# Optimization experiments

Measured on AMD Instinct MI355X. Metric: run time of the kernel, lower is better.

## Reference

```python
import jax, jax.numpy as jnp
import numpy as np

N_DYADIC = 0   # dyadic refinement order (init kwarg n)
SOLVER = 0     # first-order explicit finite-difference scheme (init kwarg solver)


def _solve_goursat(inc):
    """Solve Goursat PDE K_{p+1,q+1} = K_{p+1,q} + K_{p,q+1} - K_{p,q} + inc[p,q]*K_{p,q}
    with boundary K[0,:] = K[:,0] = 1. inc: [B, P, Q] -> returns K[P,Q] per pair: [B]."""
    B, P, Q = inc.shape
    dt = inc.dtype
    ones_b = jnp.ones((B,), dt)

    def row_step(prev_row, inc_row):
        # prev_row: [B, Q+1] = K[p, :]; inc_row: [B, Q]
        def col_step(k_left, t):
            k_diag, k_up, a = t  # K[p,q], K[p,q+1], inc[p,q], each [B]
            k_new = k_up + (k_left - k_diag) + a * k_diag
            return k_new, k_new
        xs = (prev_row[:, :-1].T, prev_row[:, 1:].T, inc_row.T)  # [Q, B] each
        _, tail = jax.lax.scan(col_step, ones_b, xs)              # tail: [Q, B]
        new_row = jnp.concatenate([ones_b[:, None], tail.T], axis=1)
        return new_row, None

    final_row, _ = jax.lax.scan(row_step, jnp.ones((B, Q + 1), dt), jnp.swapaxes(inc, 0, 1))
    return final_row[:, -1]


def _sig_kernel_gram(X, Y, n=N_DYADIC):
    """Signature-kernel Gram matrix. X: [A, M, D], Y: [B, N, D] -> [A, B]."""
    dX = X[:, 1:, :] - X[:, :-1, :]          # [A, M-1, D]
    dY = Y[:, 1:, :] - Y[:, :-1, :]          # [B, N-1, D]
    Minc = jnp.einsum('apd,bqd->abpq', dX, dY)  # pairwise increment inner products
    f = 2 ** n
    if f > 1:  # dyadic grid refinement: split each cell into f*f subcells
        Minc = jnp.repeat(jnp.repeat(Minc, f, axis=2), f, axis=3) / (f * f)
    A, B, P, Q = Minc.shape
    K = _solve_goursat(Minc.reshape(A * B, P, Q))
    return K.reshape(A, B)


def setup_inputs() -> dict:
    key = jax.random.key(0)
    kx, ky = jax.random.split(key)
    SCALE = 0.05  # small Brownian-like increments keep the exponential kernel tame
    X = jnp.cumsum(SCALE * jax.random.normal(kx, (64, 128, 64), dtype=jnp.float32), axis=1)
    Y = jnp.cumsum(SCALE * jax.random.normal(ky, (64, 128, 64), dtype=jnp.float32), axis=1)
    return {"X": X, "Y": Y}


def reference(X, Y):
    K_XX = _sig_kernel_gram(X, X)
    K_YY = _sig_kernel_gram(Y, Y)
    K_XY = _sig_kernel_gram(X, Y)
    dist = jnp.mean(K_XX) + jnp.mean(K_YY) - 2.0 * jnp.mean(K_XY)
    return jnp.mean((X[:, 0, :] - Y[:, 0, :]) ** 2) + dist
```

## Files before the change

### kernel.cpp

```cpp
#include <hip/hip_runtime.h>
#include <math.h>

#define DD 64
#define MM 128
#define PSTR 66
#define PWORDS (16 * PSTR)

typedef float  f32x4v __attribute__((ext_vector_type(4)));
typedef __bf16 bf16x8 __attribute__((ext_vector_type(8)));

#define FOR8(F) F(0) F(1) F(2) F(3) F(4) F(5) F(6) F(7)

union FragU { unsigned int u[4]; bf16x8 v; };

__device__ __forceinline__ unsigned cvtpk(float lo, float hi) {
    unsigned r;
    asm("v_cvt_pk_bf16_f32 %0, %1, %2" : "=v"(r) : "v"(lo), "v"(hi));
    return r;
}

__device__ __forceinline__ float qswap(float x) {
    int t = __builtin_amdgcn_update_dpp(0, __float_as_int(x), 0xB1, 0xF, 0xF, true);
    return __int_as_float(t);
}

__device__ __forceinline__ bf16x8 dfrag_hi(const float* __restrict__ r0,
                                           const float* __restrict__ r1) {
    float4 a0 = *(const float4*)r0, a1 = *(const float4*)(r0 + 4);
    float4 b0 = *(const float4*)r1, b1 = *(const float4*)(r1 + 4);
    FragU f;
    f.u[0] = cvtpk(b0.x - a0.x, b0.y - a0.y);
    f.u[1] = cvtpk(b0.z - a0.z, b0.w - a0.w);
    f.u[2] = cvtpk(b1.x - a1.x, b1.y - a1.y);
    f.u[3] = cvtpk(b1.z - a1.z, b1.w - a1.w);
    return f.v;
}

template<int CTRL, int RM, bool BC>
__device__ __forceinline__ float dpp_add(float x) {
    int t = __builtin_amdgcn_update_dpp(0, __float_as_int(x), CTRL, RM, 0xf, BC);
    return x + __int_as_float(t);
}

__device__ __forceinline__ void scan4(float& x0, float& x1, float& x2, float& x3) {
#define LVL(CTRL, RM, BC) \
    x0 = dpp_add<CTRL, RM, BC>(x0); \
    x1 = dpp_add<CTRL, RM, BC>(x1); \
    x2 = dpp_add<CTRL, RM, BC>(x2); \
    x3 = dpp_add<CTRL, RM, BC>(x3);
    LVL(0x111, 0xf, true)
    LVL(0x112, 0xf, true)
    LVL(0x114, 0xf, true)
    LVL(0x118, 0xf, true)
    LVL(0x142, 0xa, false)
    LVL(0x143, 0xc, false)
#undef LVL
}

__global__ __launch_bounds__(64, 2) void sig_goursat_kernel(
        const float* __restrict__ X, const float* __restrict__ Y,
        float* __restrict__ Kout)
{
#define OFFB(bb) (((((bb) >> 2) + 1)) * (2 * ((bb) >> 2) + ((bb) & 3)))
    const int t = blockIdx.x;
    int g, b, j;
    if (t < 1088) {
        g = t < 544 ? 0 : 1;
        const int u = t - g * 544;
        int bb = (int)sqrtf(8.0f * (float)u + 1.0f);
        if (bb > 63) bb = 63;
        while (bb > 0  && OFFB(bb) > u) --bb;
        while (bb < 63 && OFFB(bb + 1) <= u) ++bb;
        b = bb;
        j = u - OFFB(bb);
    } else {
        const int u = t - 1088;
        g = 2; b = u & 63; j = u >> 6;
    }
    const int a0r = 4 * j, a1r = 4 * j + 1, a2r = 4 * j + 2, a3r = 4 * j + 3;
    const bool tri = (g < 2);
    const int a0 = (tri && a0r > b) ? b : a0r;
    const int a1 = (tri && a1r > b) ? b : a1r;
    const int a2 = (tri && a2r > b) ? b : a2r;
    const int a3 = (tri && a3r > b) ? b : a3r;

    const float* __restrict__ Ub = (g == 1 ? Y : X);
    const float* __restrict__ U0 = Ub + (size_t)a0 * (MM * DD);
    const float* __restrict__ U1 = Ub + (size_t)a1 * (MM * DD);
    const float* __restrict__ U2 = Ub + (size_t)a2 * (MM * DD);
    const float* __restrict__ U3 = Ub + (size_t)a3 * (MM * DD);
    const float* __restrict__ V  = (g == 0 ? X : Y) + (size_t)b * (MM * DD);

    const int lane = threadIdx.x;
    const int l15  = lane & 15;
    const int k8   = (lane >> 4) * 8;
    const int rowg = (lane >> 4) * 4;
    const int par  = l15 & 1;

    __shared__ unsigned incL[4 * PWORDS];
    unsigned* __restrict__ pl0 = incL;
    unsigned* __restrict__ pl1 = incL + PWORDS;
    unsigned* __restrict__ pl2 = incL + 2 * PWORDS;
    unsigned* __restrict__ pl3 = incL + 3 * PWORDS;

#define TBDECL(ct) bf16x8 tb0_##ct, tb1_##ct;
    FOR8(TBDECL)
#define TBUILD(ct) { int brow_ = ct * 16 + l15; if (brow_ > 126) brow_ = 126; \
        const float* vp_ = V + (size_t)brow_ * DD + k8; \
        tb0_##ct = dfrag_hi(vp_,      vp_ + DD); \
        tb1_##ct = dfrag_hi(vp_ + 32, vp_ + DD + 32); }
    FOR8(TBUILD)

    float KL0_0 = 1.f, KL1_0 = 1.f, KL0_1 = 1.f, KL1_1 = 1.f;
    float KL0_2 = 1.f, KL1_2 = 1.f, KL0_3 = 1.f, KL1_3 = 1.f;

    const int wA = (rowg + 2 * par) * PSTR + (l15 >> 1);
    const int wB = wA + PSTR;

#define CTSTEPS(ct) { \
        f32x4v c = {0.f, 0.f, 0.f, 0.f}; \
        c = __builtin_amdgcn_mfma_f32_16x16x32_bf16(ak0_, tb0_##ct, c, 0, 0, 0); \
        c = __builtin_amdgcn_mfma_f32_16x16x32_bf16(ak1_, tb1_##ct, c, 0, 0, 0); \
        const float n0 = qswap(c[0]); const float n1 = qswap(c[1]); \
        const float n2 = qswap(c[2]); const float n3 = qswap(c[3]); \
        const float loA = par ? n2 : c[0]; const float hiA = par ? c[2] : n0; \
        const float loB = par ? n3 : c[1]; const float hiB = par ? c[3] : n1; \
        pls[wA + (ct) * 8] = cvtpk(loA, hiA); \
        pls[wB + (ct) * 8] = cvtpk(loB, hiB); }

#define STAGE1(s) { \
        const float* ap_ = U##s + aoff; \
        bf16x8 ak0_ = dfrag_hi(ap_,      ap_ + DD); \
        bf16x8 ak1_ = dfrag_hi(ap_ + 32, ap_ + DD + 32); \
        unsigned* __restrict__ pls = pl##s; \
        FOR8(CTSTEPS) }

#define SQUAD(w0_, w1_, w2_, w3_) { \
        const float iE0 = __uint_as_float((w0_) << 16); \
        const float iO0 = __uint_as_float((w0_) & 0xffff0000u); \
        const float iE1 = __uint_as_float((w1_) << 16); \
        const float iO1 = __uint_as_float((w1_) & 0xffff0000u); \
        const float iE2 = __uint_as_float((w2_) << 16); \
        const float iO2 = __uint_as_float((w2_) & 0xffff0000u); \
        const float iE3 = __uint_as_float((w3_) << 16); \
        const float iO3 = __uint_as_float((w3_) & 0xffff0000u); \
        const float m00 = iE0 * KL0_0, m10 = iO0 * KL1_0; \
        const float m01 = iE1 * KL0_1, m11 = iO1 * KL1_1; \
        const float m02 = iE2 * KL0_2, m12 = iO2 * KL1_2; \
        const float m03 = iE3 * KL0_3, m13 = iO3 * KL1_3; \
        const float q0 = m00 + m10, q1 = m01 + m11; \
        const float q2 = m02 + m12, q3 = m03 + m13; \
        float s0 = q0, s1 = q1, s2 = q2, s3 = q3; \
        scan4(s0, s1, s2, s3); \
        const float ex0 = s0 - q0, ex1 = s1 - q1; \
        const float ex2 = s2 - q2, ex3 = s3 - q3; \
        KL1_0 += ex0 + m00;  KL0_0 += ex0; \
        KL1_1 += ex1 + m01;  KL0_1 += ex1; \
        KL1_2 += ex2 + m02;  KL0_2 += ex2; \
        KL1_3 += ex3 + m03;  KL0_3 += ex3; }

    const unsigned* __restrict__ pr0 = pl0 + lane;
    const unsigned* __restrict__ pr1 = pl1 + lane;
    const unsigned* __restrict__ pr2 = pl2 + lane;
    const unsigned* __restrict__ pr3 = pl3 + lane;

    for (int band = 0; band < 8; ++band) {
        int arow = band * 16 + l15; if (arow > 126) arow = 126;
        const size_t aoff = (size_t)arow * DD + k8;
        STAGE1(0) STAGE1(1) STAGE1(2) STAGE1(3)

        unsigned e0 = pr0[0],    e1 = pr1[0],    e2 = pr2[0],    e3 = pr3[0];
        unsigned f0 = pr0[PSTR], f1 = pr1[PSTR], f2 = pr2[PSTR], f3 = pr3[PSTR];
        #pragma unroll
        for (int r = 0; r < 13; ++r) {
            unsigned n0 = pr0[(r + 2) * PSTR];
            unsigned n1 = pr1[(r + 2) * PSTR];
            unsigned n2 = pr2[(r + 2) * PSTR];
            unsigned n3 = pr3[(r + 2) * PSTR];
            SQUAD(e0, e1, e2, e3)
            e0 = f0; e1 = f1; e2 = f2; e3 = f3;
            f0 = n0; f1 = n1; f2 = n2; f3 = n3;
        }
        if (band < 7) {
            unsigned n0 = pr0[15 * PSTR], n1 = pr1[15 * PSTR];
            unsigned n2 = pr2[15 * PSTR], n3 = pr3[15 * PSTR];
            SQUAD(e0, e1, e2, e3)
            e0 = f0; e1 = f1; e2 = f2; e3 = f3;
            f0 = n0; f1 = n1; f2 = n2; f3 = n3;
            SQUAD(e0, e1, e2, e3)
            SQUAD(f0, f1, f2, f3)
        } else {
            SQUAD(e0, e1, e2, e3)
            SQUAD(f0, f1, f2, f3)
        }
    }

    if (lane == 63) {
        float* kg = Kout + (size_t)g * 4096;
        kg[a0 * 64 + b] = KL1_0;
        if (!tri || a1r <= b) kg[a1 * 64 + b] = KL1_1;
        if (!tri || a2r <= b) kg[a2 * 64 + b] = KL1_2;
        if (!tri || a3r <= b) kg[a3 * 64 + b] = KL1_3;
    }
}

__global__ void sig_reduce_kernel(const float* __restrict__ X,
                                  const float* __restrict__ Y,
                                  const float* __restrict__ Kws,
                                  float* __restrict__ out)
{
    const int t = threadIdx.x;
    double accK = 0.0, acc2 = 0.0;
    for (int i = t; i < 4096; i += 256) {
        const int a = i >> 6, b = i & 63;
        if (a <= b) {
            const double w = (a == b) ? 1.0 : 2.0;
            accK += w * (double)Kws[i];
            accK += w * (double)Kws[4096 + i];
        }
        accK -= 2.0 * (double)Kws[8192 + i];
        const float df = X[(size_t)a * (MM * DD) + b] - Y[(size_t)a * (MM * DD) + b];
        acc2 += (double)df * (double)df;
    }
    __shared__ double red[256];
    red[t] = accK / 4096.0 + acc2 / 4096.0;
    __syncthreads();
    for (int s = 128; s > 0; s >>= 1) {
        if (t < s) red[t] += red[t + s];
        __syncthreads();
    }
    if (t == 0) out[0] = (float)red[0];
}

extern "C" void kernel_launch(void* const* d_in, const int* in_sizes, int n_in,
                              void* d_out, int out_size, void* d_ws, size_t ws_size,
                              hipStream_t stream) {
    const float* X = (const float*)d_in[0];
    const float* Y = (const float*)d_in[1];
    float* Kws = (float*)d_ws;
    float* out = (float*)d_out;

    sig_goursat_kernel<<<dim3(2112), dim3(64), 0, stream>>>(X, Y, Kws);
    sig_reduce_kernel<<<dim3(1), dim3(256), 0, stream>>>(X, Y, Kws, out);
}
```

Before: 131.5 us.

## Process two Goursat pairs per wave instead of four to double grid parallelism

Each 64-thread block now solves two (a,b) signature-kernel pairs instead of four, halving per-block registers and LDS and doubling the grid. The triangular mapping is recomputed for pairs of rows, with a duplicate flag on the odd diagonal. Launch bounds rise to four blocks per unit so more waves can overlap the serial DPP scan latency. In exchange, each V-fragment load and B-side MFMA operand build is amortised over fewer pairs, and per-pair latency is unchanged.

```diff
diff --git a/kernel.cpp b/kernel.cpp
--- a/kernel.cpp
+++ b/kernel.cpp
@@ -42,12 +42,10 @@
     return x + __int_as_float(t);
 }
 
-__device__ __forceinline__ void scan4(float& x0, float& x1, float& x2, float& x3) {
+__device__ __forceinline__ void scan2(float& x0, float& x1) {
 #define LVL(CTRL, RM, BC) \
     x0 = dpp_add<CTRL, RM, BC>(x0); \
-    x1 = dpp_add<CTRL, RM, BC>(x1); \
-    x2 = dpp_add<CTRL, RM, BC>(x2); \
-    x3 = dpp_add<CTRL, RM, BC>(x3);
+    x1 = dpp_add<CTRL, RM, BC>(x1);
     LVL(0x111, 0xf, true)
     LVL(0x112, 0xf, true)
     LVL(0x114, 0xf, true)
@@ -57,39 +55,33 @@
 #undef LVL
 }
 
-__global__ __launch_bounds__(64, 2) void sig_goursat_kernel(
+__global__ __launch_bounds__(64, 4) void sig_goursat_kernel(
         const float* __restrict__ X, const float* __restrict__ Y,
         float* __restrict__ Kout)
 {
-#define OFFB(bb) (((((bb) >> 2) + 1)) * (2 * ((bb) >> 2) + ((bb) & 3)))
-    const int t = blockIdx.x;
-    int g, b, j;
-    if (t < 1088) {
-        g = t < 544 ? 0 : 1;
-        const int u = t - g * 544;
-        int bb = (int)sqrtf(8.0f * (float)u + 1.0f);
-        if (bb > 63) bb = 63;
-        while (bb > 0  && OFFB(bb) > u) --bb;
-        while (bb < 63 && OFFB(bb + 1) <= u) ++bb;
-        b = bb;
-        j = u - OFFB(bb);
+    const int bid = blockIdx.x;
+    int g, a0, a1, bcol;
+    bool dup = false;
+    if (bid < 2112) {
+        g = bid < 1056 ? 0 : 1;
+        const int t = bid - g * 1056;
+        bcol = (int)(2.0f * sqrtf((float)t + 1.0f));
+        if (bcol > 63) bcol = 63;
+        while (bcol > 0  && ((bcol + 1) * (bcol + 1)) / 4 > t) --bcol;
+        while (bcol < 63 && ((bcol + 2) * (bcol + 2)) / 4 <= t) ++bcol;
+        const int j = t - ((bcol + 1) * (bcol + 1)) / 4;
+        a0 = 2 * j; a1 = 2 * j + 1;
+        if (a1 > bcol) { a1 = a0; dup = true; }
     } else {
-        const int u = t - 1088;
-        g = 2; b = u & 63; j = u >> 6;
-    }
-    const int a0r = 4 * j, a1r = 4 * j + 1, a2r = 4 * j + 2, a3r = 4 * j + 3;
-    const bool tri = (g < 2);
-    const int a0 = (tri && a0r > b) ? b : a0r;
-    const int a1 = (tri && a1r > b) ? b : a1r;
-    const int a2 = (tri && a2r > b) ? b : a2r;
-    const int a3 = (tri && a3r > b) ? b : a3r;
+        const int t = bid - 2112;
+        g = 2; bcol = t & 63;
+        a0 = (t >> 6) * 2; a1 = a0 + 1;
+    }
 
     const float* __restrict__ Ub = (g == 1 ? Y : X);
     const float* __restrict__ U0 = Ub + (size_t)a0 * (MM * DD);
     const float* __restrict__ U1 = Ub + (size_t)a1 * (MM * DD);
-    const float* __restrict__ U2 = Ub + (size_t)a2 * (MM * DD);
-    const float* __restrict__ U3 = Ub + (size_t)a3 * (MM * DD);
-    const float* __restrict__ V  = (g == 0 ? X : Y) + (size_t)b * (MM * DD);
+    const float* __restrict__ V  = (g == 0 ? X : Y) + (size_t)bcol * (MM * DD);
 
     const int lane = threadIdx.x;
     const int l15  = lane & 15;
@@ -97,11 +89,9 @@
     const int rowg = (lane >> 4) * 4;
     const int par  = l15 & 1;
 
-    __shared__ unsigned incL[4 * PWORDS];
+    __shared__ unsigned incL[2 * PWORDS];
     unsigned* __restrict__ pl0 = incL;
     unsigned* __restrict__ pl1 = incL + PWORDS;
-    unsigned* __restrict__ pl2 = incL + 2 * PWORDS;
-    unsigned* __restrict__ pl3 = incL + 3 * PWORDS;
 
 #define TBDECL(ct) bf16x8 tb0_##ct, tb1_##ct;
     FOR8(TBDECL)
@@ -111,8 +101,8 @@
         tb1_##ct = dfrag_hi(vp_ + 32, vp_ + DD + 32); }
     FOR8(TBUILD)
 
-    float KL0_0 = 1.f, KL1_0 = 1.f, KL0_1 = 1.f, KL1_1 = 1.f;
-    float KL0_2 = 1.f, KL1_2 = 1.f, KL0_3 = 1.f, KL1_3 = 1.f;
+    float KL0_0 = 1.f, KL1_0 = 1.f;
+    float KL0_1 = 1.f, KL1_1 = 1.f;
 
     const int wA = (rowg + 2 * par) * PSTR + (l15 >> 1);
     const int wB = wA + PSTR;
@@ -135,72 +125,53 @@
         unsigned* __restrict__ pls = pl##s; \
         FOR8(CTSTEPS) }
 
-#define SQUAD(w0_, w1_, w2_, w3_) { \
+#define SDUAL(w0_, w1_) { \
         const float iE0 = __uint_as_float((w0_) << 16); \
         const float iO0 = __uint_as_float((w0_) & 0xffff0000u); \
         const float iE1 = __uint_as_float((w1_) << 16); \
         const float iO1 = __uint_as_float((w1_) & 0xffff0000u); \
-        const float iE2 = __uint_as_float((w2_) << 16); \
-        const float iO2 = __uint_as_float((w2_) & 0xffff0000u); \
-        const float iE3 = __uint_as_float((w3_) << 16); \
-        const float iO3 = __uint_as_float((w3_) & 0xffff0000u); \
         const float m00 = iE0 * KL0_0, m10 = iO0 * KL1_0; \
         const float m01 = iE1 * KL0_1, m11 = iO1 * KL1_1; \
-        const float m02 = iE2 * KL0_2, m12 = iO2 * KL1_2; \
-        const float m03 = iE3 * KL0_3, m13 = iO3 * KL1_3; \
         const float q0 = m00 + m10, q1 = m01 + m11; \
-        const float q2 = m02 + m12, q3 = m03 + m13; \
-        float s0 = q0, s1 = q1, s2 = q2, s3 = q3; \
-        scan4(s0, s1, s2, s3); \
+        float s0 = q0, s1 = q1; \
+        scan2(s0, s1); \
         const float ex0 = s0 - q0, ex1 = s1 - q1; \
-        const float ex2 = s2 - q2, ex3 = s3 - q3; \
         KL1_0 += ex0 + m00;  KL0_0 += ex0; \
-        KL1_1 += ex1 + m01;  KL0_1 += ex1; \
-        KL1_2 += ex2 + m02;  KL0_2 += ex2; \
-        KL1_3 += ex3 + m03;  KL0_3 += ex3; }
+        KL1_1 += ex1 + m01;  KL0_1 += ex1; }
 
     const unsigned* __restrict__ pr0 = pl0 + lane;
     const unsigned* __restrict__ pr1 = pl1 + lane;
-    const unsigned* __restrict__ pr2 = pl2 + lane;
-    const unsigned* __restrict__ pr3 = pl3 + lane;
 
     for (int band = 0; band < 8; ++band) {
         int arow = band * 16 + l15; if (arow > 126) arow = 126;
         const size_t aoff = (size_t)arow * DD + k8;
-        STAGE1(0) STAGE1(1) STAGE1(2) STAGE1(3)
-
-        unsigned e0 = pr0[0],    e1 = pr1[0],    e2 = pr2[0],    e3 = pr3[0];
-        unsigned f0 = pr0[PSTR], f1 = pr1[PSTR], f2 = pr2[PSTR], f3 = pr3[PSTR];
+        STAGE1(0) STAGE1(1)
+
+        unsigned e0 = pr0[0],    e1 = pr1[0];
+        unsigned f0 = pr0[PSTR], f1 = pr1[PSTR];
         #pragma unroll
         for (int r = 0; r < 13; ++r) {
             unsigned n0 = pr0[(r + 2) * PSTR];
             unsigned n1 = pr1[(r + 2) * PSTR];
-            unsigned n2 = pr2[(r + 2) * PSTR];
-            unsigned n3 = pr3[(r + 2) * PSTR];
-            SQUAD(e0, e1, e2, e3)
-            e0 = f0; e1 = f1; e2 = f2; e3 = f3;
-            f0 = n0; f1 = n1; f2 = n2; f3 = n3;
+            SDUAL(e0, e1)
+            e0 = f0; e1 = f1; f0 = n0; f1 = n1;
         }
         if (band < 7) {
             unsigned n0 = pr0[15 * PSTR], n1 = pr1[15 * PSTR];
-            unsigned n2 = pr2[15 * PSTR], n3 = pr3[15 * PSTR];
-            SQUAD(e0, e1, e2, e3)
-            e0 = f0; e1 = f1; e2 = f2; e3 = f3;
-            f0 = n0; f1 = n1; f2 = n2; f3 = n3;
-            SQUAD(e0, e1, e2, e3)
-            SQUAD(f0, f1, f2, f3)
+            SDUAL(e0, e1)
+            e0 = f0; e1 = f1; f0 = n0; f1 = n1;
+            SDUAL(e0, e1)
+            SDUAL(f0, f1)
         } else {
-            SQUAD(e0, e1, e2, e3)
-            SQUAD(f0, f1, f2, f3)
+            SDUAL(e0, e1)
+            SDUAL(f0, f1)
         }
     }
 
     if (lane == 63) {
         float* kg = Kout + (size_t)g * 4096;
-        kg[a0 * 64 + b] = KL1_0;
-        if (!tri || a1r <= b) kg[a1 * 64 + b] = KL1_1;
-        if (!tri || a2r <= b) kg[a2 * 64 + b] = KL1_2;
-        if (!tri || a3r <= b) kg[a3 * 64 + b] = KL1_3;
+        kg[a0 * 64 + bcol] = KL1_0;
+        if (!dup) kg[a1 * 64 + bcol] = KL1_1;
     }
 }
 
@@ -240,6 +211,6 @@
     float* Kws = (float*)d_ws;
     float* out = (float*)d_out;
 
-    sig_goursat_kernel<<<dim3(2112), dim3(64), 0, stream>>>(X, Y, Kws);
+    sig_goursat_kernel<<<dim3(4160), dim3(64), 0, stream>>>(X, Y, Kws);
     sig_reduce_kernel<<<dim3(1), dim3(256), 0, stream>>>(X, Y, Kws, out);
 }
```

Result: no change. 129.1 us (-1.8%).
